# Performance work log

Measured on AMD Instinct MI355X. Metric: run time of the kernel, lower is better.

Reference implementation:

```python
import jax, jax.numpy as jnp
import numpy as np

# dims
E, NB = 16, 4            # encoders, blocks per encoder
B, T = 4, 16             # batch, seq_len
DIN, DM, H = 32, 512, 512  # input dim, block state dim, block hidden
FH = 2048                # per-encoder FFNN hidden
ENC_OUT = 512            # per-encoder output dim
DEC_H, DEC_O, DEC_NH = 2048, 1024, 4  # decoder hidden, output, num hidden layers (num_layers=6 -> in + 4 hidden + out)


def setup_inputs() -> dict:
    key = jax.random.key(0)
    ks = iter(jax.random.split(key, 64))
    s = 0.02
    def p(*shape):
        return jax.random.normal(next(ks), shape, dtype=jnp.float32) * s
    inp = {
        "x": jax.random.normal(next(ks), (B, T, DIN), dtype=jnp.float32),
        # block 0 of each encoder: input = cat[x(32), state(512)] -> 544
        "e0_W0": p(E, DIN + DM, H), "e0_b0": jnp.zeros((E, H), jnp.float32),
        "e0_W1": p(E, H, H),        "e0_b1": jnp.zeros((E, H), jnp.float32),
        "e0_W2": p(E, H, DM),       "e0_b2": jnp.zeros((E, DM), jnp.float32),
        # blocks 1..3: input = cat[prev_state_out(512), state(512)] -> 1024
        "er_W0": p(NB - 1, E, 2 * DM, H), "er_b0": jnp.zeros((NB - 1, E, H), jnp.float32),
        "er_W1": p(NB - 1, E, H, H),      "er_b1": jnp.zeros((NB - 1, E, H), jnp.float32),
        "er_W2": p(NB - 1, E, H, DM),     "er_b2": jnp.zeros((NB - 1, E, DM), jnp.float32),
        # per-encoder FFNN over cat of 4 block states (4*512=2048)
        "ff_W0": p(E, NB * DM, FH), "ff_b0": jnp.zeros((E, FH), jnp.float32),
        "ff_W1": p(E, FH, ENC_OUT), "ff_b1": jnp.zeros((E, ENC_OUT), jnp.float32),
        # decoder recurrent cell: input = cat[16*512, dec_state(1024)] = 9216
        "dec_W0": p(E * ENC_OUT + DEC_O, DEC_H), "dec_b0": jnp.zeros((DEC_H,), jnp.float32),
        "dec_Wh": p(DEC_NH, DEC_H, DEC_H),       "dec_bh": jnp.zeros((DEC_NH, DEC_H), jnp.float32),
        "dec_Wo": p(DEC_H, DEC_O),               "dec_bo": jnp.zeros((DEC_O,), jnp.float32),
    }
    return inp


def reference(x, e0_W0, e0_b0, e0_W1, e0_b1, e0_W2, e0_b2,
              er_W0, er_b0, er_W1, er_b1, er_W2, er_b2,
              ff_W0, ff_b0, ff_W1, ff_b1,
              dec_W0, dec_b0, dec_Wh, dec_bh, dec_Wo, dec_bo):
    Bsz = x.shape[0]

    def elin(z, W, b):  # per-encoder batched linear: (E,B,i) @ (E,i,o)
        return jnp.einsum('ebi,eio->ebo', z, W) + b[:, None, :]

    def step(carry, x_t):
        enc_s, dec_s = carry  # enc_s: (NB,E,B,DM); dec_s: (B,DEC_O)
        xin = jnp.broadcast_to(x_t[None], (E, Bsz, DIN))
        # block 0 cell
        z = jnp.concatenate([xin, enc_s[0]], -1)
        h = jax.nn.gelu(elin(z, e0_W0, e0_b0))
        h = jax.nn.gelu(elin(h, e0_W1, e0_b1))
        s = jnp.tanh(elin(h, e0_W2, e0_b2))
        new_s = [s]
        # blocks 1..3 (fixed small structural loop)
        for r in range(NB - 1):
            z = jnp.concatenate([s, enc_s[r + 1]], -1)
            h = jax.nn.gelu(elin(z, er_W0[r], er_b0[r]))
            h = jax.nn.gelu(elin(h, er_W1[r], er_b1[r]))
            s = jnp.tanh(elin(h, er_W2[r], er_b2[r]))
            new_s.append(s)
        new_enc = jnp.stack(new_s, 0)
        # per-encoder FFNN over concatenated block states
        cat = jnp.concatenate(new_s, -1)  # (E,B,NB*DM)
        out = jax.nn.gelu(elin(cat, ff_W0, ff_b0))
        out = elin(out, ff_W1, ff_b1)     # (E,B,ENC_OUT)
        # decoder recurrent cell over cat of all encoder outputs
        dec_in = jnp.transpose(out, (1, 0, 2)).reshape(Bsz, E * ENC_OUT)
        z = jnp.concatenate([dec_in, dec_s], -1)
        h = jax.nn.gelu(z @ dec_W0 + dec_b0)
        for i in range(DEC_NH):
            h = jax.nn.gelu(h @ dec_Wh[i] + dec_bh[i])
        new_dec = jnp.tanh(h @ dec_Wo + dec_bo)
        return (new_enc, new_dec), new_dec

    enc0 = jnp.zeros((NB, E, Bsz, DM), x.dtype)
    dec0 = jnp.zeros((Bsz, DEC_O), x.dtype)
    _, ys = jax.lax.scan(step, (enc0, dec0), jnp.transpose(x, (1, 0, 2)))
    return jnp.transpose(ys, (1, 0, 2))  # (B,T,DEC_O)
```

## Files before the change

### kernel.cpp

```cpp
#include <hip/hip_runtime.h>
#include <math.h>
#include <stdint.h>

#define AG __HIP_MEMORY_SCOPE_AGENT
typedef unsigned long long ull;

__device__ __forceinline__ float ld4(const float* p) {
  return __hip_atomic_load(p, __ATOMIC_RELAXED, AG);
}
__device__ __forceinline__ void st4(float* p, float v) {
  __hip_atomic_store(p, v, __ATOMIC_RELAXED, AG);
}
__device__ __forceinline__ ull ld8(const float* p) {
  return __hip_atomic_load((const ull*)p, __ATOMIC_RELAXED, AG);
}
__device__ __forceinline__ void fence_vm() {
  asm volatile("s_waitcnt vmcnt(0)" ::: "memory");
}
__device__ __forceinline__ void waitge(unsigned* c, unsigned tgt) {
  if (threadIdx.x == 0) {
    while ((int)(__hip_atomic_load(c, __ATOMIC_RELAXED, AG) - tgt) < 0)
      __builtin_amdgcn_s_sleep(1);
  }
  __syncthreads();
}
__device__ __forceinline__ void wait_epoch(unsigned* line, unsigned epoch) {
  if (threadIdx.x == 0) {
    while ((int)(__hip_atomic_load(line, __ATOMIC_RELAXED, AG) - epoch) < 0)
      __builtin_amdgcn_s_sleep(1);
  }
  __syncthreads();
}
__device__ __forceinline__ void wr2(float* d, ull v) {
  d[0] = __uint_as_float((unsigned)v);
  d[1] = __uint_as_float((unsigned)(v >> 32));
}
__device__ __forceinline__ float act_apply(int act, float v) {
  if (act == 0) {
    float v3 = v * v * v;
    return 0.5f * v * (1.0f + tanhf(0.7978845608028654f * (v + 0.044715f * v3)));
  }
  if (act == 1) return tanhf(v);
  return v;
}

__device__ __forceinline__ void stage_signal(unsigned* stageCnt, unsigned bcT,
                                             unsigned* flag, unsigned epoch,
                                             unsigned* sflag) {
  const int tid = threadIdx.x;
  if (tid == 0) {
    unsigned old = __hip_atomic_fetch_add(stageCnt, 1u, __ATOMIC_RELAXED, AG);
    *sflag = (bcT && old == bcT - 1) ? 1u : 0u;
  }
  __syncthreads();
  if (*sflag) {
    if (tid < 64) __hip_atomic_store(flag + tid * 16, epoch, __ATOMIC_RELAXED, AG);
  }
  __syncthreads();
}

template <int KC, class ZL8, class ST>
__device__ void p4(const float* __restrict__ W, int ldw, const float* __restrict__ bias,
                   int c0, int k0, int chunk, int act, int kc, unsigned kcTgt,
                   unsigned* kcCnt, float* part,
                   unsigned* stageCnt, unsigned bcT, unsigned* flag, unsigned epoch,
                   float* lds, unsigned* sflag, ZL8&& zl8, ST&& store) {
  const int tid = threadIdx.x;
  __syncthreads();
  const int cp = chunk >> 1;
  for (int i = tid; i < 4 * cp; i += 256) {
    int b = i / cp, kp = i - b * cp;
    ull v = zl8(b, (k0 >> 1) + kp);
    wr2(&lds[b * chunk + 2 * kp], v);
  }
  __syncthreads();
  const int j = tid & 63, kq = tid >> 6;
  const int sub = chunk >> 2;
  float a0 = 0.f, a1 = 0.f, a2 = 0.f, a3 = 0.f;
  const float* wp = W + (size_t)(k0 + kq * sub) * ldw + (c0 + j);
  const float* z0 = lds + kq * sub;
  const float* z1 = z0 + chunk;
  const float* z2 = z1 + chunk;
  const float* z3 = z2 + chunk;
#pragma unroll 16
  for (int kk = 0; kk < sub; ++kk) {
    float wv = wp[(size_t)kk * ldw];
    a0 = fmaf(z0[kk], wv, a0);
    a1 = fmaf(z1[kk], wv, a1);
    a2 = fmaf(z2[kk], wv, a2);
    a3 = fmaf(z3[kk], wv, a3);
  }
  __syncthreads();
  float* red = lds;
  red[tid * 4 + 0] = a0; red[tid * 4 + 1] = a1;
  red[tid * 4 + 2] = a2; red[tid * 4 + 3] = a3;
  __syncthreads();
  const int jj = tid & 63, bb = tid >> 6;
  float v = red[jj * 4 + bb] + red[256 + jj * 4 + bb] +
            red[512 + jj * 4 + bb] + red[768 + jj * 4 + bb];
  if constexpr (KC == 1) {
    if (bias) v += bias[c0 + jj];
    v = act_apply(act, v);
    store(bb, c0 + jj, v);
    fence_vm();
    __syncthreads();
    stage_signal(stageCnt, bcT, flag, epoch, sflag);
  } else {
    st4(&part[kc * 256 + jj * 4 + bb], v);
    fence_vm();
    __syncthreads();
    if (tid == 0) {
      unsigned old = __hip_atomic_fetch_add(kcCnt, 1u, __ATOMIC_RELAXED, AG);
      *sflag = (old == kcTgt - 1) ? 1u : 0u;
    }
    __syncthreads();
    if (*sflag) {
      float s = 0.f;
#pragma unroll
      for (int q = 0; q < KC; ++q) s += ld4(&part[q * 256 + jj * 4 + bb]);
      if (bias) s += bias[c0 + jj];
      s = act_apply(act, s);
      store(bb, c0 + jj, s);
      fence_vm();
      __syncthreads();
      stage_signal(stageCnt, bcT, flag, epoch, sflag);
    }
  }
  __syncthreads();
}

template <int KC, class ZL8, class ST>
__device__ void p64(const float* __restrict__ W, int ldw, const float* __restrict__ bias,
                    int c0, int k0, int k1, int act, int kc, unsigned kcTgt,
                    unsigned* kcCnt, float* part,
                    unsigned* stageCnt, unsigned bcT, unsigned* flag, unsigned epoch,
                    float* lds, unsigned* sflag, ZL8&& zl8, ST&& store) {
  const int tid = threadIdx.x;
  const int tj = tid & 15, tr = tid >> 4;
  float acc[4][4];
#pragma unroll
  for (int r = 0; r < 4; ++r)
#pragma unroll
    for (int c = 0; c < 4; ++c) acc[r][c] = 0.f;
  float* Wl = lds;
  float* Zl = lds + 64 * 68;
  const int wk = tid >> 2, wc = (tid & 3) * 16;
  const int r1 = tid >> 3, c8 = tid & 7;
  for (int kb = k0; kb < k1; kb += 64) {
    __syncthreads();
    {
      const float* src = W + (size_t)(kb + wk) * ldw + c0 + wc;
      float4 w0 = *(const float4*)(src);
      float4 w1 = *(const float4*)(src + 4);
      float4 w2 = *(const float4*)(src + 8);
      float4 w3 = *(const float4*)(src + 12);
      *(float4*)&Wl[wk * 68 + wc + 0]  = w0;
      *(float4*)&Wl[wk * 68 + wc + 4]  = w1;
      *(float4*)&Wl[wk * 68 + wc + 8]  = w2;
      *(float4*)&Wl[wk * 68 + wc + 12] = w3;
    }
    {
      ull v[8];
#pragma unroll
      for (int q = 0; q < 8; ++q) {
        int row = (q < 4) ? r1 : 32 + r1;
        int kp = c8 + 8 * (q & 3);
        v[q] = zl8(row, (kb >> 1) + kp);
      }
#pragma unroll
      for (int q = 0; q < 8; ++q) {
        int row = (q < 4) ? r1 : 32 + r1;
        int kp = c8 + 8 * (q & 3);
        wr2(&Zl[row * 65 + 2 * kp], v[q]);
      }
    }
    __syncthreads();
#pragma unroll 4
    for (int kk = 0; kk < 64; ++kk) {
      float4 w4 = *(float4*)&Wl[kk * 68 + tj * 4];
      float zr0 = Zl[(tr * 4 + 0) * 65 + kk];
      float zr1 = Zl[(tr * 4 + 1) * 65 + kk];
      float zr2 = Zl[(tr * 4 + 2) * 65 + kk];
      float zr3 = Zl[(tr * 4 + 3) * 65 + kk];
      acc[0][0] = fmaf(zr0, w4.x, acc[0][0]); acc[0][1] = fmaf(zr0, w4.y, acc[0][1]);
      acc[0][2] = fmaf(zr0, w4.z, acc[0][2]); acc[0][3] = fmaf(zr0, w4.w, acc[0][3]);
      acc[1][0] = fmaf(zr1, w4.x, acc[1][0]); acc[1][1] = fmaf(zr1, w4.y, acc[1][1]);
      acc[1][2] = fmaf(zr1, w4.z, acc[1][2]); acc[1][3] = fmaf(zr1, w4.w, acc[1][3]);
      acc[2][0] = fmaf(zr2, w4.x, acc[2][0]); acc[2][1] = fmaf(zr2, w4.y, acc[2][1]);
      acc[2][2] = fmaf(zr2, w4.z, acc[2][2]); acc[2][3] = fmaf(zr2, w4.w, acc[2][3]);
      acc[3][0] = fmaf(zr3, w4.x, acc[3][0]); acc[3][1] = fmaf(zr3, w4.y, acc[3][1]);
      acc[3][2] = fmaf(zr3, w4.z, acc[3][2]); acc[3][3] = fmaf(zr3, w4.w, acc[3][3]);
    }
  }
  __syncthreads();
  if constexpr (KC == 1) {
#pragma unroll
    for (int r = 0; r < 4; ++r)
#pragma unroll
      for (int c = 0; c < 4; ++c) {
        int col = c0 + tj * 4 + c;
        float v = acc[r][c] + (bias ? bias[col] : 0.f);
        v = act_apply(act, v);
        store(tr * 4 + r, col, v);
      }
    fence_vm();
    __syncthreads();
    stage_signal(stageCnt, bcT, flag, epoch, sflag);
  } else {
    float* pp = part + kc * 4096;
#pragma unroll
    for (int r = 0; r < 4; ++r)
#pragma unroll
      for (int c = 0; c < 4; ++c)
        st4(&pp[(tr * 4 + r) * 64 + tj * 4 + c], acc[r][c]);
    fence_vm();
    __syncthreads();
    if (tid == 0) {
      unsigned old = __hip_atomic_fetch_add(kcCnt, 1u, __ATOMIC_RELAXED, AG);
      *sflag = (old == kcTgt - 1) ? 1u : 0u;
    }
    __syncthreads();
    if (*sflag) {
      for (int r = 0; r < 4; ++r)
        for (int c = 0; c < 4; ++c) {
          int idx = (tr * 4 + r) * 64 + tj * 4 + c;
          float s = 0.f;
#pragma unroll
          for (int q = 0; q < KC; ++q) s += ld4(&part[q * 4096 + idx]);
          int col = c0 + tj * 4 + c;
          if (bias) s += bias[col];
          s = act_apply(act, s);
          store(tr * 4 + r, col, s);
        }
      fence_vm();
      __syncthreads();
      stage_signal(stageCnt, bcT, flag, epoch, sflag);
    }
  }
  __syncthreads();
}

struct P {
  const float *x;
  const float *e0W0, *e0b0, *e0W1, *e0b1, *e0W2, *e0b2;
  const float *erW0, *erb0, *erW1, *erb1, *erW2, *erb2;
  const float *ffW0, *ffb0, *ffW1, *ffb1;
  const float *dW0, *db0, *dWh, *dbh, *dWo, *dbo;
  float *S, *h1, *h2, *g, *eo, *hd_pre, *hd0, *hd1, *dob, *pF2, *pD;
  unsigned* cnt;
  float* out;
};

#define S_IDX(r, t, e, b) ((size_t)((((r)*16 + (t)) * 16 + (e)) * 4 + (b)) * 512)

#define C_A 0
#define C_B 64
#define C_C 128
#define C_FFG 192
#define C_KF2 208
#define C_FFO 336
#define C_DC 344
#define C_KD 352
#define C_KDO 384
#define C_KL0 400
#define C_L0C 432
#define C_FFLAG 440
#define C_L0FLAG 504
#define C_OFLAG 568
#define C_DFLAG 632

__global__ __launch_bounds__(256, 2) void hrnn(P p) {
  __shared__ __align__(16) float lds[64 * 68 + 64 * 65];
  __shared__ unsigned sflag;
  const int w = blockIdx.x;
  const int e = w & 15, lvl = (w >> 4) & 3, sub = w >> 6;
  auto cptr = [&](int i) { return p.cnt + (size_t)i * 16; };
  unsigned* myline_ff = cptr(C_FFLAG + (w & 63));
  unsigned* myline_l0 = cptr(C_L0FLAG + (w & 63));
  unsigned* myline_out = cptr(C_OFLAG + (w & 63));

  {
    const float *W0, *B0, *W1, *B1, *W2, *B2;
    int K0;
    if (lvl == 0) {
      W0 = p.e0W0 + (size_t)e * 544 * 512; B0 = p.e0b0 + e * 512;
      W1 = p.e0W1 + (size_t)e * 262144;    B1 = p.e0b1 + e * 512;
      W2 = p.e0W2 + (size_t)e * 262144;    B2 = p.e0b2 + e * 512;
      K0 = 544;
    } else {
      int ri = (lvl - 1) * 16 + e;
      W0 = p.erW0 + (size_t)ri * 524288; B0 = p.erb0 + (size_t)ri * 512;
      W1 = p.erW1 + (size_t)ri * 262144; B1 = p.erb1 + (size_t)ri * 512;
      W2 = p.erW2 + (size_t)ri * 262144; B2 = p.erb2 + (size_t)ri * 512;
      K0 = 1024;
    }
    unsigned* aT = cptr(C_A + e * 4 + lvl);
    unsigned* bT = cptr(C_B + e * 4 + lvl);
    unsigned* cT = cptr(C_C + e * 4 + lvl);
    float* h1 = p.h1 + (size_t)(e * 4 + lvl) * 4 * 512;
    float* h2 = p.h2 + (size_t)(e * 4 + lvl) * 4 * 512;
    for (int t = 0; t < 16; ++t) {
      if (t) waitge(cT, 8u * t);
      if (lvl) waitge(cptr(C_C + e * 4 + lvl - 1), 8u * (t + 1));
      {
        const float* x = p.x; const float* S = p.S;
        const int tt = t, ee = e, rr = lvl;
        auto zl = [=](int b, int kp) -> ull {
          if (rr == 0) {
            if (kp < 16) return *(const ull*)(x + ((b * 16 + tt) * 32 + 2 * kp));
            return tt ? ld8(S + S_IDX(0, tt - 1, ee, b) + 2 * kp - 32) : 0ull;
          } else {
            if (kp < 256) return ld8(S + S_IDX(rr - 1, tt, ee, b) + 2 * kp);
            return tt ? ld8(S + S_IDX(rr, tt - 1, ee, b) + 2 * kp - 512) : 0ull;
          }
        };
        auto st = [=](int b, int col, float v) { st4(h1 + b * 512 + col, v); };
        p4<1>(W0, 512, B0, sub * 64, 0, K0, 0, 0, 0, nullptr, nullptr,
              aT, 0, nullptr, 0, lds, &sflag, zl, st);
      }
      waitge(aT, 8u * (t + 1));
      {
        auto zl = [=](int b, int kp) -> ull { return ld8(h1 + b * 512 + 2 * kp); };
        auto st = [=](int b, int col, float v) { st4(h2 + b * 512 + col, v); };
        p4<1>(W1, 512, B1, sub * 64, 0, 512, 0, 0, 0, nullptr, nullptr,
              bT, 0, nullptr, 0, lds, &sflag, zl, st);
      }
      waitge(bT, 8u * (t + 1));
      {
        float* S = p.S; const int tt = t, ee = e, rr = lvl;
        auto zl = [=](int b, int kp) -> ull { return ld8(h2 + b * 512 + 2 * kp); };
        auto st = [=](int b, int col, float v) { st4(S + S_IDX(rr, tt, ee, b) + col, v); };
        p4<1>(W2, 512, B2, sub * 64, 0, 512, 1, 0, 0, nullptr, nullptr,
              cT, 0, nullptr, 0, lds, &sflag, zl, st);
      }
    }
  }

  for (int r = 0; r < 4; ++r) waitge(cptr(C_C + e * 4 + r), 128u);
  {
    const float* S = p.S; const int ee = e;
    auto zl = [=](int row, int kp) -> ull {
      int k = 2 * kp, tt = row >> 2, b = row & 3, seg = k >> 9;
      return ld8(S + S_IDX(seg, tt, ee, b) + (k & 511));
    };
    float* g = p.g + (size_t)e * 131072;
    auto st = [=](int row, int col, float v) { st4(g + (size_t)row * 2048 + col, v); };
    int slot = w >> 4;
    p64<1>(p.ffW0 + (size_t)e * 4194304, 2048, p.ffb0 + e * 2048, slot * 64, 0, 2048,
           0, 0, 0, nullptr, nullptr, cptr(C_FFG + e), 0, nullptr, 0,
           lds, &sflag, zl, st);
  }
  waitge(cptr(C_FFG + e), 32u);
  {
    int ct = w >> 6, kc2 = (w >> 4) & 3;
    const float* g = p.g + (size_t)e * 131072;
    auto zl = [=](int row, int kp) -> ull { return ld8(g + (size_t)row * 2048 + 2 * kp); };
    float* eo = p.eo; const int ee = e;
    auto st = [=](int row, int col, float v) {
      int tt = row >> 2, b = row & 3;
      st4(eo + (size_t)((tt * 16 + ee) * 4 + b) * 512 + col, v);
    };
    p64<4>(p.ffW1 + (size_t)e * 1048576, 512, p.ffb1 + e * 512, ct * 64,
           kc2 * 512, (kc2 + 1) * 512, 2, kc2, 4u,
           cptr(C_KF2 + e * 8 + ct), p.pF2 + (size_t)(e * 8 + ct) * 16384,
           cptr(C_FFO), 128u, cptr(C_FFLAG), 1u, lds, &sflag, zl, st);
  }

  wait_epoch(myline_ff, 1u);
  const int tile = w >> 4, kD = w & 15;
  const int tileO = w >> 5, kO = w & 31;
  {
    const float* eo = p.eo;
    auto zl = [=](int row, int kp) -> ull {
      int k = 2 * kp, tt = row >> 2, b = row & 3, e2 = k >> 9;
      return ld8(eo + (size_t)((tt * 16 + e2) * 4 + b) * 512 + (k & 511));
    };
    float* hp = p.hd_pre;
    auto st = [=](int row, int col, float v) { st4(hp + (size_t)row * 2048 + col, v); };
    p64<16>(p.dW0, 2048, p.db0, tile * 64, kD * 512, (kD + 1) * 512, 2, kD, 16u,
            cptr(C_KL0 + tile), p.pF2 + (size_t)tile * 65536,
            cptr(C_L0C), 32u, cptr(C_L0FLAG), 1u, lds, &sflag, zl, st);
  }
  wait_epoch(myline_l0, 1u);

  {
    const float* dW0b = p.dW0 + (size_t)8192 * 2048;
    for (int t = 0; t < 16; ++t) {
      if (t) wait_epoch(myline_out, (unsigned)t);
      {
        const float* dob = p.dob; const int tt = t;
        auto zl = [=](int b, int kpg) -> ull {
          return tt ? ld8(dob + b * 1024 + 2 * kpg) : 0ull;
        };
        const float* hp = p.hd_pre; float* hd = p.hd0;
        auto st = [=](int b, int col, float v) {
          v += ld4(hp + (size_t)(tt * 4 + b) * 2048 + col);
          v = act_apply(0, v);
          st4(hd + b * 2048 + col, v);
        };
        p4<16>(dW0b, 2048, nullptr, tile * 64, kD * 64, 64, 2, kD, 80u * t + 16u,
               cptr(C_KD + tile), p.pD + (size_t)tile * 4096,
               cptr(C_DC + 0), 32u * (t + 1), cptr(C_DFLAG + 0 * 64), (unsigned)(t + 1),
               lds, &sflag, zl, st);
      }
      for (int l = 1; l <= 4; ++l) {
        wait_epoch(cptr(C_DFLAG + (l - 1) * 64 + (w & 63)), (unsigned)(t + 1));
        const float* hin = (l & 1) ? p.hd0 : p.hd1;
        float* hout = (l & 1) ? p.hd1 : p.hd0;
        auto zl = [=](int b, int kp) -> ull { return ld8(hin + b * 2048 + 2 * kp); };
        auto st = [=](int b, int col, float v) { st4(hout + b * 2048 + col, v); };
        p4<16>(p.dWh + (size_t)(l - 1) * 4194304, 2048, p.dbh + (size_t)(l - 1) * 2048,
               tile * 64, kD * 128, 128, 0, kD, 80u * t + 16u * (l + 1),
               cptr(C_KD + tile), p.pD + (size_t)tile * 4096,
               cptr(C_DC + l), 32u * (t + 1), cptr(C_DFLAG + l * 64), (unsigned)(t + 1),
               lds, &sflag, zl, st);
      }
      wait_epoch(cptr(C_DFLAG + 4 * 64 + (w & 63)), (unsigned)(t + 1));
      {
        const float* hin = p.hd0; float* dob = p.dob; float* outp = p.out; const int tt = t;
        auto zl = [=](int b, int kp) -> ull { return ld8(hin + b * 2048 + 2 * kp); };
        auto st = [=](int b, int col, float v) {
          outp[(size_t)(b * 16 + tt) * 1024 + col] = v;
          st4(dob + b * 1024 + col, v);
        };
        p4<32>(p.dWo, 1024, p.dbo, tileO * 64, kO * 64, 64, 1, kO, 32u * (t + 1),
               cptr(C_KDO + tileO), p.pD + (size_t)tileO * 8192,
               cptr(C_DC + 5), 16u * (t + 1), cptr(C_OFLAG), (unsigned)(t + 1),
               lds, &sflag, zl, st);
      }
    }
  }
}

extern "C" void kernel_launch(void* const* d_in, const int* in_sizes, int n_in,
                              void* d_out, int out_size, void* d_ws, size_t ws_size,
                              hipStream_t stream) {
  hipMemsetAsync(d_ws, 0, 65536, stream);

  P p;
  p.x    = (const float*)d_in[0];
  p.e0W0 = (const float*)d_in[1];  p.e0b0 = (const float*)d_in[2];
  p.e0W1 = (const float*)d_in[3];  p.e0b1 = (const float*)d_in[4];
  p.e0W2 = (const float*)d_in[5];  p.e0b2 = (const float*)d_in[6];
  p.erW0 = (const float*)d_in[7];  p.erb0 = (const float*)d_in[8];
  p.erW1 = (const float*)d_in[9];  p.erb1 = (const float*)d_in[10];
  p.erW2 = (const float*)d_in[11]; p.erb2 = (const float*)d_in[12];
  p.ffW0 = (const float*)d_in[13]; p.ffb0 = (const float*)d_in[14];
  p.ffW1 = (const float*)d_in[15]; p.ffb1 = (const float*)d_in[16];
  p.dW0  = (const float*)d_in[17]; p.db0  = (const float*)d_in[18];
  p.dWh  = (const float*)d_in[19]; p.dbh  = (const float*)d_in[20];
  p.dWo  = (const float*)d_in[21]; p.dbo  = (const float*)d_in[22];

  float* base = (float*)((char*)d_ws + 65536);
  p.S      = base; base += 2097152;
  p.h1     = base; base += 131072;
  p.h2     = base; base += 131072;
  p.g      = base; base += 2097152;
  p.eo     = base; base += 524288;
  p.hd_pre = base; base += 131072;
  p.hd0    = base; base += 8192;
  p.hd1    = base; base += 8192;
  p.dob    = base; base += 4096;
  p.pF2    = base; base += 2097152;
  p.pD     = base; base += 131072;

  p.cnt = (unsigned*)d_ws;
  p.out = (float*)d_out;

  hipLaunchKernelGGL(hrnn, dim3(512), dim3(256), 0, stream, p);
}
```

Before: 2.125 ms.

## Keep encoder and decoder weights resident in registers/LDS across timesteps

Restructures the persistent kernel so each workgroup holds its slice of weights in registers (encoder blocks, decoder hidden layers) or LDS (decoder input and output projections) for the whole time loop, instead of re-reading them from global memory every step. The encoder is reorganised so all 512 workgroups process one level at a time, each owning 16 columns of one encoder, and levels run one after another rather than as a pipeline. This removes repeated weight traffic but raises register pressure sharply (hundreds of floats per thread), which risks spills. It also serialises encoder levels and adds more workgroups per counter barrier.

```diff
diff --git a/kernel.cpp b/kernel.cpp
--- a/kernel.cpp
+++ b/kernel.cpp
@@ -59,72 +59,97 @@
   __syncthreads();
 }
 
-template <int KC, class ZL8, class ST>
-__device__ void p4(const float* __restrict__ W, int ldw, const float* __restrict__ bias,
-                   int c0, int k0, int chunk, int act, int kc, unsigned kcTgt,
-                   unsigned* kcCnt, float* part,
-                   unsigned* stageCnt, unsigned bcT, unsigned* flag, unsigned epoch,
-                   float* lds, unsigned* sflag, ZL8&& zl8, ST&& store) {
+template <int SUB, int K, class WF, class ZP, class ST>
+__device__ __forceinline__ void estage(WF&& wf, ZP&& zp, ST&& store,
+    const float* __restrict__ bias, int c0, int act,
+    unsigned* stageCnt, float* lds) {
   const int tid = threadIdx.x;
   __syncthreads();
-  const int cp = chunk >> 1;
-  for (int i = tid; i < 4 * cp; i += 256) {
-    int b = i / cp, kp = i - b * cp;
-    ull v = zl8(b, (k0 >> 1) + kp);
-    wr2(&lds[b * chunk + 2 * kp], v);
-  }
-  __syncthreads();
-  const int j = tid & 63, kq = tid >> 6;
-  const int sub = chunk >> 2;
+  constexpr int CP = K >> 1;
+  for (int i = tid; i < 4 * CP; i += 256) {
+    int b = i / CP, kp = i - b * CP;
+    wr2(&lds[b * K + 2 * kp], zp(b, kp));
+  }
+  __syncthreads();
+  const int kq = tid >> 4;
   float a0 = 0.f, a1 = 0.f, a2 = 0.f, a3 = 0.f;
-  const float* wp = W + (size_t)(k0 + kq * sub) * ldw + (c0 + j);
-  const float* z0 = lds + kq * sub;
-  const float* z1 = z0 + chunk;
-  const float* z2 = z1 + chunk;
-  const float* z3 = z2 + chunk;
-#pragma unroll 16
-  for (int kk = 0; kk < sub; ++kk) {
-    float wv = wp[(size_t)kk * ldw];
-    a0 = fmaf(z0[kk], wv, a0);
-    a1 = fmaf(z1[kk], wv, a1);
-    a2 = fmaf(z2[kk], wv, a2);
-    a3 = fmaf(z3[kk], wv, a3);
+  const float* zq = lds + kq * SUB;
+#pragma unroll
+  for (int kk = 0; kk < SUB; ++kk) {
+    float wv = wf(kk);
+    a0 = fmaf(zq[kk], wv, a0);
+    a1 = fmaf(zq[K + kk], wv, a1);
+    a2 = fmaf(zq[2 * K + kk], wv, a2);
+    a3 = fmaf(zq[3 * K + kk], wv, a3);
   }
   __syncthreads();
   float* red = lds;
   red[tid * 4 + 0] = a0; red[tid * 4 + 1] = a1;
   red[tid * 4 + 2] = a2; red[tid * 4 + 3] = a3;
   __syncthreads();
+  if (tid < 64) {
+    const int c2 = tid >> 2, b = tid & 3;
+    float v = 0.f;
+#pragma unroll
+    for (int g = 0; g < 16; ++g) v += red[g * 64 + c2 * 4 + b];
+    v += bias[c0 + c2];
+    v = act_apply(act, v);
+    store(b, c0 + c2, v);
+  }
+  fence_vm();
+  __syncthreads();
+  if (tid == 0) __hip_atomic_fetch_add(stageCnt, 1u, __ATOMIC_RELAXED, AG);
+  __syncthreads();
+}
+
+template <int SUB, int KC, class WF, class ZP, class FIN>
+__device__ __forceinline__ void rstage(WF&& wf, ZP&& zp, FIN&& fin,
+    float* part, unsigned* kcCnt, unsigned kcTgt, int kc,
+    unsigned* stageCnt, unsigned bcT, unsigned* flag, unsigned epoch,
+    float* lds, unsigned* sflag) {
+  const int tid = threadIdx.x;
+  const int kq = tid >> 6;
+  constexpr int CH = 4 * SUB;
+  __syncthreads();
+  for (int i = tid; i < 2 * CH; i += 256) {
+    int b = i / (CH / 2), kp = i - b * (CH / 2);
+    wr2(&lds[b * CH + 2 * kp], zp(b, kp));
+  }
+  __syncthreads();
+  float a0 = 0.f, a1 = 0.f, a2 = 0.f, a3 = 0.f;
+  const float* z0 = lds + kq * SUB;
+#pragma unroll
+  for (int kk = 0; kk < SUB; ++kk) {
+    float wv = wf(kk);
+    a0 = fmaf(z0[kk], wv, a0);
+    a1 = fmaf(z0[CH + kk], wv, a1);
+    a2 = fmaf(z0[2 * CH + kk], wv, a2);
+    a3 = fmaf(z0[3 * CH + kk], wv, a3);
+  }
+  __syncthreads();
+  float* red = lds;
+  red[tid * 4 + 0] = a0; red[tid * 4 + 1] = a1;
+  red[tid * 4 + 2] = a2; red[tid * 4 + 3] = a3;
+  __syncthreads();
   const int jj = tid & 63, bb = tid >> 6;
   float v = red[jj * 4 + bb] + red[256 + jj * 4 + bb] +
             red[512 + jj * 4 + bb] + red[768 + jj * 4 + bb];
-  if constexpr (KC == 1) {
-    if (bias) v += bias[c0 + jj];
-    v = act_apply(act, v);
-    store(bb, c0 + jj, v);
+  st4(&part[kc * 256 + jj * 4 + bb], v);
+  fence_vm();
+  __syncthreads();
+  if (tid == 0) {
+    unsigned old = __hip_atomic_fetch_add(kcCnt, 1u, __ATOMIC_RELAXED, AG);
+    *sflag = (old == kcTgt - 1) ? 1u : 0u;
+  }
+  __syncthreads();
+  if (*sflag) {
+    float s = 0.f;
+#pragma unroll
+    for (int q = 0; q < KC; ++q) s += ld4(&part[q * 256 + jj * 4 + bb]);
+    fin(bb, jj, s);
     fence_vm();
     __syncthreads();
     stage_signal(stageCnt, bcT, flag, epoch, sflag);
-  } else {
-    st4(&part[kc * 256 + jj * 4 + bb], v);
-    fence_vm();
-    __syncthreads();
-    if (tid == 0) {
-      unsigned old = __hip_atomic_fetch_add(kcCnt, 1u, __ATOMIC_RELAXED, AG);
-      *sflag = (old == kcTgt - 1) ? 1u : 0u;
-    }
-    __syncthreads();
-    if (*sflag) {
-      float s = 0.f;
-#pragma unroll
-      for (int q = 0; q < KC; ++q) s += ld4(&part[q * 256 + jj * 4 + bb]);
-      if (bias) s += bias[c0 + jj];
-      s = act_apply(act, s);
-      store(bb, c0 + jj, s);
-      fence_vm();
-      __syncthreads();
-      stage_signal(stageCnt, bcT, flag, epoch, sflag);
-    }
   }
   __syncthreads();
 }
@@ -270,73 +295,95 @@
 #define C_DFLAG 632
 
 __global__ __launch_bounds__(256, 2) void hrnn(P p) {
-  __shared__ __align__(16) float lds[64 * 68 + 64 * 65];
+  __shared__ __align__(16) float lds[8512];
+  __shared__ __align__(16) float wlds[8192];
   __shared__ unsigned sflag;
   const int w = blockIdx.x;
-  const int e = w & 15, lvl = (w >> 4) & 3, sub = w >> 6;
+  const int tid = threadIdx.x;
+  const int e = w & 15;
   auto cptr = [&](int i) { return p.cnt + (size_t)i * 16; };
   unsigned* myline_ff = cptr(C_FFLAG + (w & 63));
   unsigned* myline_l0 = cptr(C_L0FLAG + (w & 63));
   unsigned* myline_out = cptr(C_OFLAG + (w & 63));
 
   {
-    const float *W0, *B0, *W1, *B1, *W2, *B2;
-    int K0;
-    if (lvl == 0) {
-      W0 = p.e0W0 + (size_t)e * 544 * 512; B0 = p.e0b0 + e * 512;
-      W1 = p.e0W1 + (size_t)e * 262144;    B1 = p.e0b1 + e * 512;
-      W2 = p.e0W2 + (size_t)e * 262144;    B2 = p.e0b2 + e * 512;
-      K0 = 544;
-    } else {
-      int ri = (lvl - 1) * 16 + e;
-      W0 = p.erW0 + (size_t)ri * 524288; B0 = p.erb0 + (size_t)ri * 512;
-      W1 = p.erW1 + (size_t)ri * 262144; B1 = p.erb1 + (size_t)ri * 512;
-      W2 = p.erW2 + (size_t)ri * 262144; B2 = p.erb2 + (size_t)ri * 512;
-      K0 = 1024;
-    }
-    unsigned* aT = cptr(C_A + e * 4 + lvl);
-    unsigned* bT = cptr(C_B + e * 4 + lvl);
-    unsigned* cT = cptr(C_C + e * 4 + lvl);
-    float* h1 = p.h1 + (size_t)(e * 4 + lvl) * 4 * 512;
-    float* h2 = p.h2 + (size_t)(e * 4 + lvl) * 4 * 512;
-    for (int t = 0; t < 16; ++t) {
-      if (t) waitge(cT, 8u * t);
-      if (lvl) waitge(cptr(C_C + e * 4 + lvl - 1), 8u * (t + 1));
-      {
-        const float* x = p.x; const float* S = p.S;
-        const int tt = t, ee = e, rr = lvl;
-        auto zl = [=](int b, int kp) -> ull {
+    const int cs = w >> 4;
+    const int c0e = cs * 16;
+    const int ekq = tid >> 4, ec = tid & 15;
+    float w0r[64], w1r[32], w2r[32];
+    float* h1 = p.h1 + (size_t)e * 2048;
+    float* h2 = p.h2 + (size_t)e * 2048;
+    for (int lvl = 0; lvl < 4; ++lvl) {
+      const float *W0, *B0, *W1, *B1, *W2, *B2;
+      if (lvl == 0) {
+        W0 = p.e0W0 + (size_t)e * 544 * 512; B0 = p.e0b0 + e * 512;
+        W1 = p.e0W1 + (size_t)e * 262144;    B1 = p.e0b1 + e * 512;
+        W2 = p.e0W2 + (size_t)e * 262144;    B2 = p.e0b2 + e * 512;
+      } else {
+        int ri = (lvl - 1) * 16 + e;
+        W0 = p.erW0 + (size_t)ri * 524288; B0 = p.erb0 + (size_t)ri * 512;
+        W1 = p.erW1 + (size_t)ri * 262144; B1 = p.erb1 + (size_t)ri * 512;
+        W2 = p.erW2 + (size_t)ri * 262144; B2 = p.erb2 + (size_t)ri * 512;
+      }
+      if (lvl == 0) {
+#pragma unroll
+        for (int kk = 0; kk < 34; ++kk)
+          w0r[kk] = W0[(size_t)(ekq * 34 + kk) * 512 + c0e + ec];
+      } else {
+#pragma unroll
+        for (int kk = 0; kk < 64; ++kk)
+          w0r[kk] = W0[(size_t)(ekq * 64 + kk) * 512 + c0e + ec];
+      }
+#pragma unroll
+      for (int kk = 0; kk < 32; ++kk) {
+        w1r[kk] = W1[(size_t)(ekq * 32 + kk) * 512 + c0e + ec];
+        w2r[kk] = W2[(size_t)(ekq * 32 + kk) * 512 + c0e + ec];
+      }
+      unsigned* aT = cptr(C_A + e * 4 + lvl);
+      unsigned* bT = cptr(C_B + e * 4 + lvl);
+      unsigned* cT = cptr(C_C + e * 4 + lvl);
+      if (lvl) waitge(cptr(C_C + e * 4 + lvl - 1), 512u);
+      auto wfa = [&](int kk) { return w0r[kk]; };
+      auto wfb = [&](int kk) { return w1r[kk]; };
+      auto wfc = [&](int kk) { return w2r[kk]; };
+      for (int t = 0; t < 16; ++t) {
+        if (t) waitge(cT, 32u * t);
+        {
+          const float* x = p.x; const float* S = p.S;
+          const int tt = t, ee = e, rr = lvl;
+          auto st = [=](int b, int col, float v) { st4(h1 + b * 512 + col, v); };
           if (rr == 0) {
-            if (kp < 16) return *(const ull*)(x + ((b * 16 + tt) * 32 + 2 * kp));
-            return tt ? ld8(S + S_IDX(0, tt - 1, ee, b) + 2 * kp - 32) : 0ull;
+            auto zp = [=](int b, int kp) -> ull {
+              if (kp < 16) return *(const ull*)(x + ((b * 16 + tt) * 32 + 2 * kp));
+              return tt ? ld8(S + S_IDX(0, tt - 1, ee, b) + 2 * kp - 32) : 0ull;
+            };
+            estage<34, 544>(wfa, zp, st, B0, c0e, 0, aT, lds);
           } else {
-            if (kp < 256) return ld8(S + S_IDX(rr - 1, tt, ee, b) + 2 * kp);
-            return tt ? ld8(S + S_IDX(rr, tt - 1, ee, b) + 2 * kp - 512) : 0ull;
+            auto zp = [=](int b, int kp) -> ull {
+              if (kp < 256) return ld8(S + S_IDX(rr - 1, tt, ee, b) + 2 * kp);
+              return tt ? ld8(S + S_IDX(rr, tt - 1, ee, b) + 2 * kp - 512) : 0ull;
+            };
+            estage<64, 1024>(wfa, zp, st, B0, c0e, 0, aT, lds);
           }
-        };
-        auto st = [=](int b, int col, float v) { st4(h1 + b * 512 + col, v); };
-        p4<1>(W0, 512, B0, sub * 64, 0, K0, 0, 0, 0, nullptr, nullptr,
-              aT, 0, nullptr, 0, lds, &sflag, zl, st);
-      }
-      waitge(aT, 8u * (t + 1));
-      {
-        auto zl = [=](int b, int kp) -> ull { return ld8(h1 + b * 512 + 2 * kp); };
-        auto st = [=](int b, int col, float v) { st4(h2 + b * 512 + col, v); };
-        p4<1>(W1, 512, B1, sub * 64, 0, 512, 0, 0, 0, nullptr, nullptr,
-              bT, 0, nullptr, 0, lds, &sflag, zl, st);
-      }
-      waitge(bT, 8u * (t + 1));
-      {
-        float* S = p.S; const int tt = t, ee = e, rr = lvl;
-        auto zl = [=](int b, int kp) -> ull { return ld8(h2 + b * 512 + 2 * kp); };
-        auto st = [=](int b, int col, float v) { st4(S + S_IDX(rr, tt, ee, b) + col, v); };
-        p4<1>(W2, 512, B2, sub * 64, 0, 512, 1, 0, 0, nullptr, nullptr,
-              cT, 0, nullptr, 0, lds, &sflag, zl, st);
-      }
-    }
-  }
-
-  for (int r = 0; r < 4; ++r) waitge(cptr(C_C + e * 4 + r), 128u);
+        }
+        waitge(aT, 32u * (t + 1));
+        {
+          auto zp = [=](int b, int kp) -> ull { return ld8(h1 + b * 512 + 2 * kp); };
+          auto st = [=](int b, int col, float v) { st4(h2 + b * 512 + col, v); };
+          estage<32, 512>(wfb, zp, st, B1, c0e, 0, bT, lds);
+        }
+        waitge(bT, 32u * (t + 1));
+        {
+          float* S = p.S; const int tt = t, ee = e, rr = lvl;
+          auto zp = [=](int b, int kp) -> ull { return ld8(h2 + b * 512 + 2 * kp); };
+          auto st = [=](int b, int col, float v) { st4(S + S_IDX(rr, tt, ee, b) + col, v); };
+          estage<32, 512>(wfc, zp, st, B2, c0e, 1, cT, lds);
+        }
+      }
+    }
+  }
+
+  for (int r = 0; r < 4; ++r) waitge(cptr(C_C + e * 4 + r), 512u);
   {
     const float* S = p.S; const int ee = e;
     auto zl = [=](int row, int kp) -> ull {
@@ -381,53 +428,83 @@
             cptr(C_KL0 + tile), p.pF2 + (size_t)tile * 65536,
             cptr(C_L0C), 32u, cptr(C_L0FLAG), 1u, lds, &sflag, zl, st);
   }
+
+  const int dj = tid & 63, dkq = tid >> 6;
+  for (int i = tid; i < 4096; i += 256) {
+    int kl = i >> 6, j2 = i & 63;
+    wlds[i]        = p.dW0[(size_t)(8192 + kD * 64 + kl) * 2048 + tile * 64 + j2];
+    wlds[4096 + i] = p.dWo[(size_t)(kO * 64 + kl) * 1024 + tileO * 64 + j2];
+  }
+  float whr0[32], whr1[32], whr2[32], whr3[32];
+#pragma unroll
+  for (int kk = 0; kk < 32; ++kk)
+    whr0[kk] = p.dWh[((size_t)(0 * 2048 + kD * 128 + dkq * 32 + kk)) * 2048 + tile * 64 + dj];
+#pragma unroll
+  for (int kk = 0; kk < 32; ++kk)
+    whr1[kk] = p.dWh[((size_t)(1 * 2048 + kD * 128 + dkq * 32 + kk)) * 2048 + tile * 64 + dj];
+#pragma unroll
+  for (int kk = 0; kk < 32; ++kk)
+    whr2[kk] = p.dWh[((size_t)(2 * 2048 + kD * 128 + dkq * 32 + kk)) * 2048 + tile * 64 + dj];
+#pragma unroll
+  for (int kk = 0; kk < 32; ++kk)
+    whr3[kk] = p.dWh[((size_t)(3 * 2048 + kD * 128 + dkq * 32 + kk)) * 2048 + tile * 64 + dj];
+  __syncthreads();
   wait_epoch(myline_l0, 1u);
 
-  {
-    const float* dW0b = p.dW0 + (size_t)8192 * 2048;
-    for (int t = 0; t < 16; ++t) {
-      if (t) wait_epoch(myline_out, (unsigned)t);
-      {
-        const float* dob = p.dob; const int tt = t;
-        auto zl = [=](int b, int kpg) -> ull {
-          return tt ? ld8(dob + b * 1024 + 2 * kpg) : 0ull;
-        };
-        const float* hp = p.hd_pre; float* hd = p.hd0;
-        auto st = [=](int b, int col, float v) {
-          v += ld4(hp + (size_t)(tt * 4 + b) * 2048 + col);
-          v = act_apply(0, v);
-          st4(hd + b * 2048 + col, v);
-        };
-        p4<16>(dW0b, 2048, nullptr, tile * 64, kD * 64, 64, 2, kD, 80u * t + 16u,
-               cptr(C_KD + tile), p.pD + (size_t)tile * 4096,
-               cptr(C_DC + 0), 32u * (t + 1), cptr(C_DFLAG + 0 * 64), (unsigned)(t + 1),
-               lds, &sflag, zl, st);
-      }
-      for (int l = 1; l <= 4; ++l) {
-        wait_epoch(cptr(C_DFLAG + (l - 1) * 64 + (w & 63)), (unsigned)(t + 1));
-        const float* hin = (l & 1) ? p.hd0 : p.hd1;
-        float* hout = (l & 1) ? p.hd1 : p.hd0;
-        auto zl = [=](int b, int kp) -> ull { return ld8(hin + b * 2048 + 2 * kp); };
-        auto st = [=](int b, int col, float v) { st4(hout + b * 2048 + col, v); };
-        p4<16>(p.dWh + (size_t)(l - 1) * 4194304, 2048, p.dbh + (size_t)(l - 1) * 2048,
-               tile * 64, kD * 128, 128, 0, kD, 80u * t + 16u * (l + 1),
-               cptr(C_KD + tile), p.pD + (size_t)tile * 4096,
-               cptr(C_DC + l), 32u * (t + 1), cptr(C_DFLAG + l * 64), (unsigned)(t + 1),
-               lds, &sflag, zl, st);
-      }
-      wait_epoch(cptr(C_DFLAG + 4 * 64 + (w & 63)), (unsigned)(t + 1));
-      {
-        const float* hin = p.hd0; float* dob = p.dob; float* outp = p.out; const int tt = t;
-        auto zl = [=](int b, int kp) -> ull { return ld8(hin + b * 2048 + 2 * kp); };
-        auto st = [=](int b, int col, float v) {
-          outp[(size_t)(b * 16 + tt) * 1024 + col] = v;
-          st4(dob + b * 1024 + col, v);
-        };
-        p4<32>(p.dWo, 1024, p.dbo, tileO * 64, kO * 64, 64, 1, kO, 32u * (t + 1),
-               cptr(C_KDO + tileO), p.pD + (size_t)tileO * 8192,
-               cptr(C_DC + 5), 16u * (t + 1), cptr(C_OFLAG), (unsigned)(t + 1),
-               lds, &sflag, zl, st);
-      }
+  auto layer = [&](int l, const float (&whr)[32], const float* hin, float* hout,
+                   int t) __attribute__((always_inline)) {
+    wait_epoch(cptr(C_DFLAG + (l - 1) * 64 + (w & 63)), (unsigned)(t + 1));
+    auto wf = [&](int kk) { return whr[kk]; };
+    auto zp = [&](int b, int kp) -> ull { return ld8(hin + b * 2048 + 2 * (kD * 64 + kp)); };
+    const float* dbh = p.dbh + (size_t)(l - 1) * 2048;
+    const int c0d = tile * 64;
+    auto fin = [&](int bb, int jj, float s) {
+      int col = c0d + jj; s += dbh[col]; s = act_apply(0, s);
+      st4(hout + bb * 2048 + col, s);
+    };
+    rstage<32, 16>(wf, zp, fin, p.pD + (size_t)tile * 4096, cptr(C_KD + tile),
+                   80u * t + 16u * (l + 1), kD, cptr(C_DC + l), 32u * (t + 1),
+                   cptr(C_DFLAG + l * 64), (unsigned)(t + 1), lds, &sflag);
+  };
+
+  for (int t = 0; t < 16; ++t) {
+    if (t) wait_epoch(myline_out, (unsigned)t);
+    {
+      float* dob = p.dob; const int tt = t;
+      auto wf = [&](int kk) { return wlds[(dkq * 16 + kk) * 64 + dj]; };
+      auto zp = [&](int b, int kp) -> ull {
+        return tt ? ld8(dob + b * 1024 + 2 * (kD * 32 + kp)) : 0ull;
+      };
+      const float* hp = p.hd_pre; float* hd0 = p.hd0; const int c0d = tile * 64;
+      auto fin = [&](int bb, int jj, float s) {
+        int col = c0d + jj;
+        s += ld4(hp + (size_t)(tt * 4 + bb) * 2048 + col);
+        s = act_apply(0, s);
+        st4(hd0 + bb * 2048 + col, s);
+      };
+      rstage<16, 16>(wf, zp, fin, p.pD + (size_t)tile * 4096, cptr(C_KD + tile),
+                     80u * t + 16u, kD, cptr(C_DC + 0), 32u * (t + 1),
+                     cptr(C_DFLAG + 0 * 64), (unsigned)(t + 1), lds, &sflag);
+    }
+    layer(1, whr0, p.hd0, p.hd1, t);
+    layer(2, whr1, p.hd1, p.hd0, t);
+    layer(3, whr2, p.hd0, p.hd1, t);
+    layer(4, whr3, p.hd1, p.hd0, t);
+    wait_epoch(cptr(C_DFLAG + 4 * 64 + (w & 63)), (unsigned)(t + 1));
+    {
+      auto wf = [&](int kk) { return wlds[4096 + (dkq * 16 + kk) * 64 + dj]; };
+      float* hd0 = p.hd0;
+      auto zp = [&](int b, int kp) -> ull { return ld8(hd0 + b * 2048 + 2 * (kO * 32 + kp)); };
+      const float* dbo = p.dbo; float* outp = p.out; float* dob = p.dob;
+      const int c0o = tileO * 64; const int tt = t;
+      auto fin = [&](int bb, int jj, float s) {
+        int col = c0o + jj; s += dbo[col]; s = tanhf(s);
+        outp[(size_t)(bb * 16 + tt) * 1024 + col] = s;
+        st4(dob + bb * 1024 + col, s);
+      };
+      rstage<16, 32>(wf, zp, fin, p.pD + (size_t)tileO * 8192, cptr(C_KDO + tileO),
+                     32u * (t + 1), kO, cptr(C_DC + 5), 16u * (t + 1),
+                     cptr(C_OFLAG), (unsigned)(t + 1), lds, &sflag);
     }
   }
 }
@@ -453,8 +530,8 @@
 
   float* base = (float*)((char*)d_ws + 65536);
   p.S      = base; base += 2097152;
-  p.h1     = base; base += 131072;
-  p.h2     = base; base += 131072;
+  p.h1     = base; base += 32768;
+  p.h2     = base; base += 32768;
   p.g      = base; base += 2097152;
   p.eo     = base; base += 524288;
   p.hd_pre = base; base += 131072;
```

Result: slower. 3.106 ms (+46.2%).
